# Optimization experiments

Measured on AMD Instinct MI355X. Metric: run time of the kernel, lower is better.

Reference implementation:

```python
import jax, jax.numpy as jnp
import numpy as np

N_NODES = 65536
N_EDGES = 1048576
D_IN = 1024
D_HID = 64
N_CLS = 32


def gcn_conv(x, W, b, src, dst, n_nodes):
    """PyG GCNConv: linear transform, then symmetric-normalized aggregation
    with implicit self-loops (fill value 1)."""
    xw = x @ W  # [N, d_out]
    e = src.shape[0]
    # degree over destination index, including the self-loop (+1)
    deg = jax.ops.segment_sum(jnp.ones((e,), xw.dtype), dst, num_segments=n_nodes) + 1.0
    dinv_sqrt = jax.lax.rsqrt(deg)  # deg >= 1, safe
    norm = dinv_sqrt[src] * dinv_sqrt[dst]  # [E]
    agg = jax.ops.segment_sum(xw[src] * norm[:, None], dst, num_segments=n_nodes)
    # self-loop contribution: norm = deg_i^{-1}
    agg = agg + xw * (1.0 / deg)[:, None]
    return agg + b


def setup_inputs() -> dict:
    key = jax.random.key(0)
    k_x, k_e, k_w1, k_b1, k_w2, k_b2 = jax.random.split(key, 6)
    x = jax.random.normal(k_x, (N_NODES, D_IN), dtype=jnp.float32)
    edge_index = jax.random.randint(k_e, (2, N_EDGES), 0, N_NODES, dtype=jnp.int64)
    s1 = 1.0 / np.sqrt(D_IN)
    s2 = 1.0 / np.sqrt(D_HID)
    W1 = jax.random.uniform(k_w1, (D_IN, D_HID), jnp.float32, -s1, s1)
    b1 = jax.random.uniform(k_b1, (D_HID,), jnp.float32, -s1, s1)
    W2 = jax.random.uniform(k_w2, (D_HID, N_CLS), jnp.float32, -s2, s2)
    b2 = jax.random.uniform(k_b2, (N_CLS,), jnp.float32, -s2, s2)
    return {"x": x, "edge_index": edge_index, "W1": W1, "b1": b1, "W2": W2, "b2": b2}


def reference(x, edge_index, W1, b1, W2, b2):
    src, dst = edge_index[0], edge_index[1]
    n = x.shape[0]
    h = gcn_conv(x, W1, b1, src, dst, n)
    h = jax.nn.relu(h)
    # dropout is identity in eval mode
    h = gcn_conv(h, W2, b2, src, dst, n)
    return jax.nn.log_softmax(h, axis=1)
```

## Files before the change

kernel.cpp:

```cpp
#include <hip/hip_runtime.h>
#include <hip/hip_bf16.h>

#define N_NODES 65536
#define D_IN 1024
#define D_HID 64
#define N_CLS 32

typedef short short8 __attribute__((ext_vector_type(8)));
typedef float floatx4 __attribute__((ext_vector_type(4)));

__device__ __forceinline__ unsigned short f2bf(float f) {
  union { float f; unsigned u; } cv; cv.f = f;
  unsigned r = (cv.u + 0x7FFFu + ((cv.u >> 16) & 1u)) >> 16;
  return (unsigned short)r;
}
__device__ __forceinline__ float2 bf2f2(unsigned v) {
  union { unsigned u; float f; } a, b;
  a.u = v << 16;
  b.u = v & 0xFFFF0000u;
  return make_float2(a.f, b.f);
}

__global__ void k_count_w1t(const int* __restrict__ dst, int* __restrict__ cnt,
                            const float* __restrict__ w1, unsigned short* __restrict__ w1t,
                            int e4) {
  int b = blockIdx.x;
  if (b >= 1024) {
    int i = (b - 1024) * 256 + threadIdx.x;
    int k = i / D_HID, n = i % D_HID;
    w1t[n * D_IN + k] = f2bf(w1[i]);
    return;
  }
  int i = b * 256 + threadIdx.x;
  if (i < e4) {
    int4 d = ((const int4*)dst)[i];
    atomicAdd(&cnt[d.x], 1);
    atomicAdd(&cnt[d.y], 1);
    atomicAdd(&cnt[d.z], 1);
    atomicAdd(&cnt[d.w], 1);
  }
}

__global__ void k_scan_a(const int* __restrict__ cnt, int* __restrict__ bsum) {
  __shared__ int s[256];
  int t = threadIdx.x;
  s[t] = cnt[blockIdx.x * 256 + t];
  __syncthreads();
  for (int off = 128; off > 0; off >>= 1) {
    if (t < off) s[t] += s[t + off];
    __syncthreads();
  }
  if (t == 0) bsum[blockIdx.x] = s[0];
}

__global__ void k_scan_c(const int* __restrict__ cnt, const int* __restrict__ bsum,
                         int* __restrict__ rowptr, int* __restrict__ cursor,
                         float* __restrict__ dinv) {
  __shared__ int s[256];
  int t = threadIdx.x;
  s[t] = (t < blockIdx.x) ? bsum[t] : 0;
  __syncthreads();
  for (int off = 128; off > 0; off >>= 1) {
    if (t < off) s[t] += s[t + off];
    __syncthreads();
  }
  int blockoff = s[0];
  __syncthreads();
  int i = blockIdx.x * 256 + t;
  int v = cnt[i];
  s[t] = v;
  __syncthreads();
  for (int off = 1; off < 256; off <<= 1) {
    int x = (t >= off) ? s[t - off] : 0;
    __syncthreads();
    s[t] += x;
    __syncthreads();
  }
  int excl = s[t] - v + blockoff;
  rowptr[i] = excl;
  cursor[i] = excl;
  dinv[i] = rsqrtf((float)(v + 1));
  if (i == N_NODES - 1) rowptr[N_NODES] = excl + v;
}

__global__ __launch_bounds__(256) void k_fill_gemm1(
    const int* __restrict__ src, const int* __restrict__ dst,
    int* __restrict__ cursor, int* __restrict__ csr_src, int e4,
    const float* __restrict__ x, const unsigned short* __restrict__ w1t,
    const float* __restrict__ dinv, unsigned short* __restrict__ xw1s) {
  if (blockIdx.x >= 1024) {
    int i = (blockIdx.x - 1024) * 256 + threadIdx.x;
    if (i < e4) {
      int4 d = ((const int4*)dst)[i];
      int4 s = ((const int4*)src)[i];
      csr_src[atomicAdd(&cursor[d.x], 1)] = s.x;
      csr_src[atomicAdd(&cursor[d.y], 1)] = s.y;
      csr_src[atomicAdd(&cursor[d.z], 1)] = s.z;
      csr_src[atomicAdd(&cursor[d.w], 1)] = s.w;
    }
    return;
  }
  int wave = threadIdx.x >> 6;
  int lane = threadIdx.x & 63;
  int quad = lane >> 4;
  int l16 = lane & 15;
  int rowbase = blockIdx.x * 64 + wave * 16;
  const float* xrow = x + (size_t)(rowbase + l16) * D_IN + quad * 8;
  const unsigned short* bbase = w1t + quad * 8;
  floatx4 acc[4];
#pragma unroll
  for (int nt = 0; nt < 4; nt++) acc[nt] = (floatx4){0.f, 0.f, 0.f, 0.f};
  float4 p0 = *(const float4*)(xrow + 0);
  float4 p1 = *(const float4*)(xrow + 4);
  float4 p2 = *(const float4*)(xrow + 32);
  float4 p3 = *(const float4*)(xrow + 36);
  for (int k0 = 0; k0 < D_IN; k0 += 64) {
    float4 c0 = p0, c1 = p1, c2 = p2, c3 = p3;
    if (k0 + 64 < D_IN) {
      p0 = *(const float4*)(xrow + k0 + 64);
      p1 = *(const float4*)(xrow + k0 + 68);
      p2 = *(const float4*)(xrow + k0 + 96);
      p3 = *(const float4*)(xrow + k0 + 100);
    }
    float av0[8] = {c0.x, c0.y, c0.z, c0.w, c1.x, c1.y, c1.z, c1.w};
    float av1[8] = {c2.x, c2.y, c2.z, c2.w, c3.x, c3.y, c3.z, c3.w};
    short8 af0, af1;
#pragma unroll
    for (int j = 0; j < 8; j++) { af0[j] = (short)f2bf(av0[j]); af1[j] = (short)f2bf(av1[j]); }
    short8 bf0[4], bf1[4];
#pragma unroll
    for (int nt = 0; nt < 4; nt++) {
      const unsigned short* bp = bbase + (size_t)(nt * 16 + l16) * D_IN + k0;
      bf0[nt] = *(const short8*)(bp);
      bf1[nt] = *(const short8*)(bp + 32);
    }
#pragma unroll
    for (int nt = 0; nt < 4; nt++)
      acc[nt] = __builtin_amdgcn_mfma_f32_16x16x32_bf16(af0, bf0[nt], acc[nt], 0, 0, 0);
#pragma unroll
    for (int nt = 0; nt < 4; nt++)
      acc[nt] = __builtin_amdgcn_mfma_f32_16x16x32_bf16(af1, bf1[nt], acc[nt], 0, 0, 0);
  }
#pragma unroll
  for (int r = 0; r < 4; r++) {
    int row = rowbase + quad * 4 + r;
    float sc = dinv[row];
#pragma unroll
    for (int nt = 0; nt < 4; nt++)
      xw1s[(size_t)row * D_HID + nt * 16 + l16] = f2bf(acc[nt][r] * sc);
  }
}

__global__ __launch_bounds__(256) void k_agg1(const unsigned* __restrict__ xw1s2,
    const int* __restrict__ rowptr, const int* __restrict__ csr_src,
    const float* __restrict__ dinv, const float* __restrict__ b1,
    const float* __restrict__ w2, unsigned short* __restrict__ xw2s) {
  __shared__ float w2s[D_HID * N_CLS];
  __shared__ float2 hbuf[4][32];
  for (int i = threadIdx.x; i < D_HID * N_CLS; i += 256) w2s[i] = w2[i];
  __syncthreads();
  int wave = threadIdx.x >> 6;
  int lane = threadIdx.x & 63;
  int h = lane >> 5, l = lane & 31;
  int node = blockIdx.x * 4 + wave;
  float dd = dinv[node];
  int beg = rowptr[node], end = rowptr[node + 1];
  float cx[8], cy[8];
#pragma unroll
  for (int j = 0; j < 8; j++) { cx[j] = 0.f; cy[j] = 0.f; }
  int e = beg + h;
  for (; e + 14 < end; e += 16) {
    int idx[8];
#pragma unroll
    for (int j = 0; j < 8; j++) idx[j] = csr_src[e + 2 * j];
#pragma unroll
    for (int j = 0; j < 8; j++) {
      float2 v = bf2f2(xw1s2[(size_t)idx[j] * 32 + l]);
      cx[j] += v.x; cy[j] += v.y;
    }
  }
  for (; e < end; e += 2) {
    float2 v = bf2f2(xw1s2[(size_t)csr_src[e] * 32 + l]);
    cx[0] += v.x; cy[0] += v.y;
  }
  float sx = ((cx[0] + cx[1]) + (cx[2] + cx[3])) + ((cx[4] + cx[5]) + (cx[6] + cx[7]));
  float sy = ((cy[0] + cy[1]) + (cy[2] + cy[3])) + ((cy[4] + cy[5]) + (cy[6] + cy[7]));
  sx += __shfl_down(sx, 32);
  sy += __shfl_down(sy, 32);
  if (lane < 32) {
    float2 self = bf2f2(xw1s2[(size_t)node * 32 + l]);
    float2 bb = ((const float2*)b1)[l];
    float vx = dd * (sx + self.x) + bb.x;
    float vy = dd * (sy + self.y) + bb.y;
    hbuf[wave][l] = make_float2(vx > 0.f ? vx : 0.f, vy > 0.f ? vy : 0.f);
  }
  __syncthreads();
  const float* hb = (const float*)hbuf[wave];
  int c = lane & 31;
  float p = 0.f;
#pragma unroll
  for (int kk = 0; kk < 32; kk++) {
    int k = h * 32 + kk;
    p += hb[k] * w2s[k * N_CLS + c];
  }
  p += __shfl_down(p, 32);
  if (lane < 32) xw2s[(size_t)node * N_CLS + c] = f2bf(p * dd);
}

__global__ __launch_bounds__(256) void k_agg2(const unsigned* __restrict__ xw2s2,
    const int* __restrict__ rowptr, const int* __restrict__ csr_src,
    const float* __restrict__ dinv, const float* __restrict__ b2,
    float* __restrict__ out) {
  int wave = threadIdx.x >> 6;
  int lane = threadIdx.x & 63;
  int q = lane >> 4, l = lane & 15;
  int node = blockIdx.x * 4 + wave;
  float dd = dinv[node];
  int beg = rowptr[node], end = rowptr[node + 1];
  float cx[4], cy[4];
#pragma unroll
  for (int j = 0; j < 4; j++) { cx[j] = 0.f; cy[j] = 0.f; }
  int e = beg + q;
  for (; e + 12 < end; e += 16) {
    int idx[4];
#pragma unroll
    for (int j = 0; j < 4; j++) idx[j] = csr_src[e + 4 * j];
#pragma unroll
    for (int j = 0; j < 4; j++) {
      float2 v = bf2f2(xw2s2[(size_t)idx[j] * 16 + l]);
      cx[j] += v.x; cy[j] += v.y;
    }
  }
  for (; e < end; e += 4) {
    float2 v = bf2f2(xw2s2[(size_t)csr_src[e] * 16 + l]);
    cx[0] += v.x; cy[0] += v.y;
  }
  float sx = (cx[0] + cx[1]) + (cx[2] + cx[3]);
  float sy = (cy[0] + cy[1]) + (cy[2] + cy[3]);
  sx += __shfl_down(sx, 32); sy += __shfl_down(sy, 32);
  sx += __shfl_down(sx, 16); sy += __shfl_down(sy, 16);
  if (lane < 16) {
    float2 self = bf2f2(xw2s2[(size_t)node * 16 + l]);
    float2 bb = ((const float2*)b2)[l];
    float lx = dd * (sx + self.x) + bb.x;
    float ly = dd * (sy + self.y) + bb.y;
    float m = fmaxf(lx, ly);
#pragma unroll
    for (int o = 8; o > 0; o >>= 1) m = fmaxf(m, __shfl_xor(m, o));
    float s2 = __expf(lx - m) + __expf(ly - m);
#pragma unroll
    for (int o = 8; o > 0; o >>= 1) s2 += __shfl_xor(s2, o);
    float lse = m + __logf(s2);
    ((float2*)out)[(size_t)node * 16 + l] = make_float2(lx - lse, ly - lse);
  }
}

extern "C" void kernel_launch(void* const* d_in, const int* in_sizes, int n_in,
                              void* d_out, int out_size, void* d_ws, size_t ws_size,
                              hipStream_t stream) {
  (void)n_in; (void)out_size; (void)ws_size;
  const float* x  = (const float*)d_in[0];
  const int*   ei = (const int*)d_in[1];
  const float* w1 = (const float*)d_in[2];
  const float* b1 = (const float*)d_in[3];
  const float* w2 = (const float*)d_in[4];
  const float* b2 = (const float*)d_in[5];
  float* out = (float*)d_out;
  int e = in_sizes[1] / 2;
  const int* src = ei;
  const int* dst = ei + e;

  char* ws = (char*)d_ws;
  int* cnt            = (int*)(ws + 0x000000);
  int* rowptr         = (int*)(ws + 0x040000);
  int* cursor         = (int*)(ws + 0x0C0000);
  float* dinv         = (float*)(ws + 0x100000);
  int* bsum           = (int*)(ws + 0x140000);
  int* csr_src        = (int*)(ws + 0x180000);
  unsigned short* w1t = (unsigned short*)(ws + 0x580000);
  unsigned short* xw1s= (unsigned short*)(ws + 0x600000);
  unsigned short* xw2s= (unsigned short*)(ws + 0xE00000);

  int e4 = e / 4;
  hipMemsetAsync(cnt, 0, N_NODES * sizeof(int), stream);
  k_count_w1t<<<1280, 256, 0, stream>>>(dst, cnt, w1, w1t, e4);
  k_scan_a   <<<N_NODES / 256, 256, 0, stream>>>(cnt, bsum);
  k_scan_c   <<<N_NODES / 256, 256, 0, stream>>>(cnt, bsum, rowptr, cursor, dinv);
  k_fill_gemm1<<<2048, 256, 0, stream>>>(src, dst, cursor, csr_src, e4,
                                         x, w1t, dinv, xw1s);
  k_agg1     <<<N_NODES / 4, 256, 0, stream>>>((const unsigned*)xw1s, rowptr, csr_src,
                                               dinv, b1, w2, xw2s);
  k_agg2     <<<N_NODES / 4, 256, 0, stream>>>((const unsigned*)xw2s, rowptr, csr_src,
                                               dinv, b2, out);
}
```

Measured before the change: 564.1 us.

## Batch CSR fill atomics, use packed bf16 convert, predicate gather tails, shuffle-based hidden broadcast

The CSR fill path now has each thread handle eight edges and issue all atomics before the stores, so atomic latency overlaps; grid shrinks to match. The GEMM's software bf16 rounding is replaced by the hardware packed-convert instruction. Both aggregation kernels drop the scalar tail loop in favour of a predicated unrolled loop. agg1 replaces its shared-memory hidden buffer and block barrier with wave shuffles. These target atomic latency, ALU cost of conversion, tail divergence and sync overhead, at the cost of extra predicated loads and many shuffles.

```diff
diff --git a/kernel.cpp b/kernel.cpp
--- a/kernel.cpp
+++ b/kernel.cpp
@@ -90,13 +90,24 @@
     const float* __restrict__ dinv, unsigned short* __restrict__ xw1s) {
   if (blockIdx.x >= 1024) {
     int i = (blockIdx.x - 1024) * 256 + threadIdx.x;
-    if (i < e4) {
-      int4 d = ((const int4*)dst)[i];
-      int4 s = ((const int4*)src)[i];
-      csr_src[atomicAdd(&cursor[d.x], 1)] = s.x;
-      csr_src[atomicAdd(&cursor[d.y], 1)] = s.y;
-      csr_src[atomicAdd(&cursor[d.z], 1)] = s.z;
-      csr_src[atomicAdd(&cursor[d.w], 1)] = s.w;
+    int e8 = e4 >> 1;
+    if (i < e8) {
+      const int4* d4 = (const int4*)dst;
+      const int4* s4 = (const int4*)src;
+      int4 da = d4[2 * i], db = d4[2 * i + 1];
+      int4 sa = s4[2 * i], sb = s4[2 * i + 1];
+      int p0 = atomicAdd(&cursor[da.x], 1);
+      int p1 = atomicAdd(&cursor[da.y], 1);
+      int p2 = atomicAdd(&cursor[da.z], 1);
+      int p3 = atomicAdd(&cursor[da.w], 1);
+      int p4 = atomicAdd(&cursor[db.x], 1);
+      int p5 = atomicAdd(&cursor[db.y], 1);
+      int p6 = atomicAdd(&cursor[db.z], 1);
+      int p7 = atomicAdd(&cursor[db.w], 1);
+      csr_src[p0] = sa.x; csr_src[p1] = sa.y;
+      csr_src[p2] = sa.z; csr_src[p3] = sa.w;
+      csr_src[p4] = sb.x; csr_src[p5] = sb.y;
+      csr_src[p6] = sb.z; csr_src[p7] = sb.w;
     }
     return;
   }
@@ -125,8 +136,13 @@
     float av0[8] = {c0.x, c0.y, c0.z, c0.w, c1.x, c1.y, c1.z, c1.w};
     float av1[8] = {c2.x, c2.y, c2.z, c2.w, c3.x, c3.y, c3.z, c3.w};
     short8 af0, af1;
-#pragma unroll
-    for (int j = 0; j < 8; j++) { af0[j] = (short)f2bf(av0[j]); af1[j] = (short)f2bf(av1[j]); }
+    unsigned* u0 = (unsigned*)&af0;
+    unsigned* u1 = (unsigned*)&af1;
+#pragma unroll
+    for (int j = 0; j < 4; j++) {
+      asm("v_cvt_pk_bf16_f32 %0, %1, %2" : "=v"(u0[j]) : "v"(av0[2 * j]), "v"(av0[2 * j + 1]));
+      asm("v_cvt_pk_bf16_f32 %0, %1, %2" : "=v"(u1[j]) : "v"(av1[2 * j]), "v"(av1[2 * j + 1]));
+    }
     short8 bf0[4], bf1[4];
 #pragma unroll
     for (int nt = 0; nt < 4; nt++) {
@@ -156,7 +172,6 @@
     const float* __restrict__ dinv, const float* __restrict__ b1,
     const float* __restrict__ w2, unsigned short* __restrict__ xw2s) {
   __shared__ float w2s[D_HID * N_CLS];
-  __shared__ float2 hbuf[4][32];
   for (int i = threadIdx.x; i < D_HID * N_CLS; i += 256) w2s[i] = w2[i];
   __syncthreads();
   int wave = threadIdx.x >> 6;
@@ -168,42 +183,40 @@
   float cx[8], cy[8];
 #pragma unroll
   for (int j = 0; j < 8; j++) { cx[j] = 0.f; cy[j] = 0.f; }
-  int e = beg + h;
-  for (; e + 14 < end; e += 16) {
-    int idx[8];
-#pragma unroll
-    for (int j = 0; j < 8; j++) idx[j] = csr_src[e + 2 * j];
+  for (int e = beg + h; e < end; e += 16) {
+    int idx[8]; bool val[8];
+#pragma unroll
+    for (int j = 0; j < 8; j++) {
+      int ee = e + 2 * j;
+      val[j] = ee < end;
+      idx[j] = csr_src[val[j] ? ee : beg];
+    }
 #pragma unroll
     for (int j = 0; j < 8; j++) {
       float2 v = bf2f2(xw1s2[(size_t)idx[j] * 32 + l]);
-      cx[j] += v.x; cy[j] += v.y;
-    }
-  }
-  for (; e < end; e += 2) {
-    float2 v = bf2f2(xw1s2[(size_t)csr_src[e] * 32 + l]);
-    cx[0] += v.x; cy[0] += v.y;
+      cx[j] += val[j] ? v.x : 0.f;
+      cy[j] += val[j] ? v.y : 0.f;
+    }
   }
   float sx = ((cx[0] + cx[1]) + (cx[2] + cx[3])) + ((cx[4] + cx[5]) + (cx[6] + cx[7]));
   float sy = ((cy[0] + cy[1]) + (cy[2] + cy[3])) + ((cy[4] + cy[5]) + (cy[6] + cy[7]));
-  sx += __shfl_down(sx, 32);
-  sy += __shfl_down(sy, 32);
-  if (lane < 32) {
-    float2 self = bf2f2(xw1s2[(size_t)node * 32 + l]);
-    float2 bb = ((const float2*)b1)[l];
-    float vx = dd * (sx + self.x) + bb.x;
-    float vy = dd * (sy + self.y) + bb.y;
-    hbuf[wave][l] = make_float2(vx > 0.f ? vx : 0.f, vy > 0.f ? vy : 0.f);
-  }
-  __syncthreads();
-  const float* hb = (const float*)hbuf[wave];
+  sx += __shfl_xor(sx, 32);
+  sy += __shfl_xor(sy, 32);
+  float2 self = bf2f2(xw1s2[(size_t)node * 32 + l]);
+  float2 bb = ((const float2*)b1)[l];
+  float vx = dd * (sx + self.x) + bb.x;
+  float vy = dd * (sy + self.y) + bb.y;
+  vx = vx > 0.f ? vx : 0.f;
+  vy = vy > 0.f ? vy : 0.f;
   int c = lane & 31;
   float p = 0.f;
 #pragma unroll
   for (int kk = 0; kk < 32; kk++) {
     int k = h * 32 + kk;
-    p += hb[k] * w2s[k * N_CLS + c];
-  }
-  p += __shfl_down(p, 32);
+    float hv = (k & 1) ? __shfl(vy, k >> 1) : __shfl(vx, k >> 1);
+    p += hv * w2s[k * N_CLS + c];
+  }
+  p += __shfl_xor(p, 32);
   if (lane < 32) xw2s[(size_t)node * N_CLS + c] = f2bf(p * dd);
 }
 
@@ -220,39 +233,38 @@
   float cx[4], cy[4];
 #pragma unroll
   for (int j = 0; j < 4; j++) { cx[j] = 0.f; cy[j] = 0.f; }
-  int e = beg + q;
-  for (; e + 12 < end; e += 16) {
-    int idx[4];
-#pragma unroll
-    for (int j = 0; j < 4; j++) idx[j] = csr_src[e + 4 * j];
+  for (int e = beg + q; e < end; e += 16) {
+    int idx[4]; bool val[4];
+#pragma unroll
+    for (int j = 0; j < 4; j++) {
+      int ee = e + 4 * j;
+      val[j] = ee < end;
+      idx[j] = csr_src[val[j] ? ee : beg];
+    }
 #pragma unroll
     for (int j = 0; j < 4; j++) {
       float2 v = bf2f2(xw2s2[(size_t)idx[j] * 16 + l]);
-      cx[j] += v.x; cy[j] += v.y;
-    }
-  }
-  for (; e < end; e += 4) {
-    float2 v = bf2f2(xw2s2[(size_t)csr_src[e] * 16 + l]);
-    cx[0] += v.x; cy[0] += v.y;
+      cx[j] += val[j] ? v.x : 0.f;
+      cy[j] += val[j] ? v.y : 0.f;
+    }
   }
   float sx = (cx[0] + cx[1]) + (cx[2] + cx[3]);
   float sy = (cy[0] + cy[1]) + (cy[2] + cy[3]);
-  sx += __shfl_down(sx, 32); sy += __shfl_down(sy, 32);
-  sx += __shfl_down(sx, 16); sy += __shfl_down(sy, 16);
-  if (lane < 16) {
-    float2 self = bf2f2(xw2s2[(size_t)node * 16 + l]);
-    float2 bb = ((const float2*)b2)[l];
-    float lx = dd * (sx + self.x) + bb.x;
-    float ly = dd * (sy + self.y) + bb.y;
-    float m = fmaxf(lx, ly);
-#pragma unroll
-    for (int o = 8; o > 0; o >>= 1) m = fmaxf(m, __shfl_xor(m, o));
-    float s2 = __expf(lx - m) + __expf(ly - m);
-#pragma unroll
-    for (int o = 8; o > 0; o >>= 1) s2 += __shfl_xor(s2, o);
-    float lse = m + __logf(s2);
+  sx += __shfl_xor(sx, 32); sy += __shfl_xor(sy, 32);
+  sx += __shfl_xor(sx, 16); sy += __shfl_xor(sy, 16);
+  float2 self = bf2f2(xw2s2[(size_t)node * 16 + l]);
+  float2 bb = ((const float2*)b2)[l];
+  float lx = dd * (sx + self.x) + bb.x;
+  float ly = dd * (sy + self.y) + bb.y;
+  float m = fmaxf(lx, ly);
+#pragma unroll
+  for (int o = 8; o > 0; o >>= 1) m = fmaxf(m, __shfl_xor(m, o));
+  float s2 = __expf(lx - m) + __expf(ly - m);
+#pragma unroll
+  for (int o = 8; o > 0; o >>= 1) s2 += __shfl_xor(s2, o);
+  float lse = m + __logf(s2);
+  if (lane < 16)
     ((float2*)out)[(size_t)node * 16 + l] = make_float2(lx - lse, ly - lse);
-  }
 }
 
 extern "C" void kernel_launch(void* const* d_in, const int* in_sizes, int n_in,
@@ -286,7 +298,7 @@
   k_count_w1t<<<1280, 256, 0, stream>>>(dst, cnt, w1, w1t, e4);
   k_scan_a   <<<N_NODES / 256, 256, 0, stream>>>(cnt, bsum);
   k_scan_c   <<<N_NODES / 256, 256, 0, stream>>>(cnt, bsum, rowptr, cursor, dinv);
-  k_fill_gemm1<<<2048, 256, 0, stream>>>(src, dst, cursor, csr_src, e4,
+  k_fill_gemm1<<<1536, 256, 0, stream>>>(src, dst, cursor, csr_src, e4,
                                          x, w1t, dinv, xw1s);
   k_agg1     <<<N_NODES / 4, 256, 0, stream>>>((const unsigned*)xw1s, rowptr, csr_src,
                                                dinv, b1, w2, xw2s);
```

Result: faster. 553.0 us (-2.0%).
